# Kernel optimization log

Measured on AMD Instinct MI355X. Metric: run time of the kernel, lower is better.

Reference implementation:

```python
import jax, jax.numpy as jnp
import numpy as np

D_MODEL = 1024
NUM_HEADS = 16
HEAD_DIM = D_MODEL // NUM_HEADS
WINDOW = 64
GLOBAL_TOKENS = 4
MAX_SEQ_LEN = 2048
RANDOM_TOKENS = 32
BATCH = 2
SEQ = 2048
NEG = -1.0e9
LN_EPS = 1e-5


def setup_inputs() -> dict:
    key = jax.random.key(0)
    k1, k2, k3, k4 = jax.random.split(key, 4)
    x = jax.random.normal(k1, (BATCH, SEQ, D_MODEL), dtype=jnp.float32)
    w_qkv = jax.random.normal(k2, (D_MODEL, 3 * D_MODEL), dtype=jnp.float32) * (D_MODEL ** -0.5)
    w_out = jax.random.normal(k3, (D_MODEL, D_MODEL), dtype=jnp.float32) * (D_MODEL ** -0.5)
    ln_gamma = jnp.ones((D_MODEL,), dtype=jnp.float32)
    ln_beta = jnp.zeros((D_MODEL,), dtype=jnp.float32)
    rand_idx = jax.random.randint(k4, (MAX_SEQ_LEN, RANDOM_TOKENS), 0, MAX_SEQ_LEN, dtype=jnp.int32)
    return {"x": x, "w_qkv": w_qkv, "w_out": w_out,
            "ln_gamma": ln_gamma, "ln_beta": ln_beta, "rand_idx": rand_idx}


def _build_masks(seq_len, rand_idx):
    i = jnp.arange(seq_len)
    causal = (i[:, None] >= i[None, :]).astype(jnp.float32)  # [L,L], lower-triangular
    # local window mask
    dist = jnp.abs(i[:, None] - i[None, :])
    local = (dist <= WINDOW).astype(jnp.float32) * causal
    # global column mask: columns {0..G-1} u {L-G..L-1}, rows i >= g (== causal on those cols)
    gcols = jnp.concatenate([jnp.arange(GLOBAL_TOKENS), jnp.arange(seq_len - GLOBAL_TOKENS, seq_len)])
    is_gcol = jnp.zeros((seq_len,), jnp.float32).at[gcols].set(1.0)
    glob = is_gcol[None, :] * causal
    # random mask: per-row fixed random columns, then causal-filtered
    ri = rand_idx[:seq_len]  # [L, R]
    rows = jnp.broadcast_to(i[:, None], ri.shape)
    rnd = jnp.zeros((seq_len, seq_len), jnp.float32).at[rows, ri].set(1.0) * causal
    return local, glob, rnd


def reference(x, w_qkv, w_out, ln_gamma, ln_beta, rand_idx):
    B, L, _ = x.shape
    residual = x
    # LayerNorm
    mu = jnp.mean(x, axis=-1, keepdims=True)
    var = jnp.mean(jnp.square(x - mu), axis=-1, keepdims=True)
    xn = (x - mu) * jax.lax.rsqrt(var + LN_EPS) * ln_gamma + ln_beta
    # QKV projection
    qkv = xn @ w_qkv
    q, k, v = jnp.split(qkv, 3, axis=-1)
    q = q.reshape(B, L, NUM_HEADS, HEAD_DIM).transpose(0, 2, 1, 3)  # [B,H,L,D]
    k = k.reshape(B, L, NUM_HEADS, HEAD_DIM).transpose(0, 2, 1, 3)
    v = v.reshape(B, L, NUM_HEADS, HEAD_DIM).transpose(0, 2, 1, 3)
    local, glob, rnd = _build_masks(L, rand_idx)
    raw = jnp.einsum('bhqd,bhkd->bhqk', q, k) / jnp.sqrt(jnp.float32(HEAD_DIM))
    # original sums three masked copies of the same scores:
    # combined = 3*raw + ((1-local)+(1-glob)+(1-rnd)) * NEG
    penalty = (3.0 - (local + glob + rnd)) * NEG  # [L,L]
    combined = 3.0 * raw + penalty[None, None, :, :]
    attn = jax.nn.softmax(combined, axis=-1)
    out = jnp.einsum('bhqk,bhkd->bhqd', attn, v)
    out = out.transpose(0, 2, 1, 3).reshape(B, L, D_MODEL)
    out = out @ w_out
    return out + residual
```

## Files before the change

kernel.cpp:

```cpp
#include <hip/hip_runtime.h>
#include <stdint.h>

typedef __attribute__((ext_vector_type(8))) short shortx8;
typedef __attribute__((ext_vector_type(4))) float floatx4;

static constexpr int SEQ_    = 2048;
static constexpr int DMODEL  = 1024;
static constexpr int HDIM    = 64;
static constexpr int BATCH_  = 2;
static constexpr int NHEADS  = 16;
static constexpr int WINDOW_ = 64;
static constexpr int GTOK    = 4;
static constexpr int RTOK    = 32;
static constexpr int ROWS    = BATCH_ * SEQ_;
static constexpr int QKVN    = 3 * DMODEL;

__device__ inline unsigned short f2bf(float f) {
  union { float f; unsigned int u; } x; x.f = f;
  unsigned int r = (x.u + 0x7FFFu + ((x.u >> 16) & 1u)) >> 16;
  return (unsigned short)r;
}
__device__ inline float bf2f(unsigned short b) {
  union { unsigned int u; float f; } x; x.u = ((unsigned int)b) << 16;
  return x.f;
}

__device__ inline void gload_lds16(const void* g, void* l) {
  __builtin_amdgcn_global_load_lds(
      (const __attribute__((address_space(1))) void*)g,
      (__attribute__((address_space(3))) void*)l, 16, 0, 0);
}

__device__ __forceinline__ void gemm_core_k1024(
    const unsigned short* __restrict__ aSrc0, const unsigned short* __restrict__ aSrc1,
    const unsigned short* __restrict__ bSrc,
    unsigned short* Al, unsigned short* Bl,
    const int wave, const int lane, floatx4 (&acc)[4][2]) {
  const int quad = lane >> 4, l16 = lane & 15;
  const int wm = (wave >> 1) * 64, wn = (wave & 1) * 32;
  unsigned short* AlD0 = Al + (wave * 32) * 32;
  unsigned short* AlD1 = Al + (wave * 32 + 16) * 32;
  unsigned short* BlD  = Bl + (wave * 16) * 32;
  for (int k0 = 0; k0 < 1024; k0 += 32) {
    __syncthreads();
    gload_lds16(aSrc0 + k0, AlD0);
    gload_lds16(aSrc1 + k0, AlD1);
    gload_lds16(bSrc  + k0, BlD);
    __syncthreads();
    shortx8 af[4], bfr[2];
    #pragma unroll
    for (int s = 0; s < 4; s++)
      af[s] = *(const shortx8*)&Al[(wm + s * 16 + l16) * 32 + quad * 8];
    #pragma unroll
    for (int s = 0; s < 2; s++)
      bfr[s] = *(const shortx8*)&Bl[(wn + s * 16 + l16) * 32 + quad * 8];
    #pragma unroll
    for (int sm = 0; sm < 4; sm++)
      #pragma unroll
      for (int sn = 0; sn < 2; sn++)
        acc[sm][sn] = __builtin_amdgcn_mfma_f32_16x16x32_bf16(af[sm], bfr[sn], acc[sm][sn], 0, 0, 0);
  }
}

__global__ __launch_bounds__(256) void k1_prep(
    const float* __restrict__ x, const float* __restrict__ w_qkv,
    const float* __restrict__ w_out, const float* __restrict__ gamma,
    const float* __restrict__ beta, const int* __restrict__ ridx,
    unsigned short* __restrict__ xn, unsigned short* __restrict__ wqT,
    unsigned short* __restrict__ woT, unsigned short* __restrict__ Wvs,
    int* __restrict__ cols, int* __restrict__ cnt, int* __restrict__ tmx,
    int* __restrict__ cnts2, int* __restrict__ qlist) {
  __shared__ float tile[32][33];
  __shared__ float red[4], red2[4];
  __shared__ int rl[RTOK];
  __shared__ int scw, scnw, stm;
  const int bx = blockIdx.x;
  const int t = threadIdx.x;
  if (bx < 3072) {
    int n0 = (bx % 96) * 32, k0 = (bx / 96) * 32;
    int tx = t & 31, ty = t >> 5;
    #pragma unroll
    for (int r = ty; r < 32; r += 8)
      tile[r][tx] = w_qkv[(size_t)(k0 + r) * QKVN + n0 + tx];
    __syncthreads();
    #pragma unroll
    for (int r = ty; r < 32; r += 8)
      wqT[(size_t)(n0 + r) * DMODEL + k0 + tx] = f2bf(tile[tx][r]);
  } else if (bx < 7168) {
    int row = bx - 3072;
    const float4* xr = (const float4*)(x + (size_t)row * DMODEL);
    float4 v = xr[t];
    float s = v.x + v.y + v.z + v.w;
    #pragma unroll
    for (int o = 32; o > 0; o >>= 1) s += __shfl_xor(s, o);
    int wave = t >> 6, lane = t & 63;
    if (lane == 0) red[wave] = s;
    __syncthreads();
    float mean = (red[0] + red[1] + red[2] + red[3]) * (1.0f / DMODEL);
    float dx = v.x - mean, dy = v.y - mean, dz = v.z - mean, dw = v.w - mean;
    float q = dx*dx + dy*dy + dz*dz + dw*dw;
    #pragma unroll
    for (int o = 32; o > 0; o >>= 1) q += __shfl_xor(q, o);
    if (lane == 0) red2[wave] = q;
    __syncthreads();
    float var = (red2[0] + red2[1] + red2[2] + red2[3]) * (1.0f / DMODEL);
    float rs = rsqrtf(var + 1e-5f);
    float4 g = ((const float4*)gamma)[t];
    float4 bb = ((const float4*)beta)[t];
    ushort4 outv;
    outv.x = f2bf(dx * rs * g.x + bb.x);
    outv.y = f2bf(dy * rs * g.y + bb.y);
    outv.z = f2bf(dz * rs * g.z + bb.z);
    outv.w = f2bf(dw * rs * g.w + bb.w);
    ((ushort4*)(xn + (size_t)row * DMODEL))[t] = outv;
  } else if (bx < 8192) {
    int idx = bx - 7168;
    int n0 = (idx & 31) * 32, k0 = (idx >> 5) * 32;
    int tx = t & 31, ty = t >> 5;
    #pragma unroll
    for (int r = ty; r < 32; r += 8)
      tile[r][tx] = w_out[(size_t)(k0 + r) * DMODEL + n0 + tx];
    __syncthreads();
    #pragma unroll
    for (int r = ty; r < 32; r += 8)
      woT[(size_t)(n0 + r) * DMODEL + k0 + tx] = f2bf(tile[tx][r]);
  } else if (bx < 9216) {
    int idx = bx - 8192;
    int v0 = (idx & 31) * 32, k0 = (idx >> 5) * 32;
    int tx = t & 31, ty = t >> 5;
    #pragma unroll
    for (int r = ty; r < 32; r += 8)
      Wvs[(size_t)(k0 + r) * DMODEL + v0 + tx] =
          f2bf(w_qkv[(size_t)(k0 + r) * QKVN + 2 * DMODEL + v0 + tx]);
  } else {
    const int i = bx - 9216;
    if (t < RTOK) rl[t] = ridx[i * RTOK + t];
    if (t == 0) { scw = 0; scnw = 0; stm = 0; }
    __syncthreads();
    const int wstart = (i - WINDOW_ > 0) ? (i - WINDOW_) : 0;
    const int c = t;
    int j = -1;
    bool valid = false;
    bool iswin = (c < 65);
    if (c < 65) {
      j = i - WINDOW_ + c;
      valid = (j >= 0);
    } else if (c < 73) {
      int g = c - 65;
      j = (g < 4) ? g : (SEQ_ - 8 + g);
      valid = (j <= i) && (j < wstart);
    } else if (c < 73 + RTOK) {
      int r = c - 73;
      j = rl[r];
      bool dup = false;
      for (int r2 = 0; r2 < r; r2++) dup = dup || (rl[r2] == j);
      valid = (j <= i) && (j < wstart) && !(j < GTOK || j >= SEQ_ - GTOK) && !dup;
    }
    int tier = -1;
    if (valid) {
      int loc = ((i - j) <= WINDOW_) ? 1 : 0;
      int glb = (j < GTOK || j >= SEQ_ - GTOK) ? 1 : 0;
      int rnd = 0;
      for (int r = 0; r < RTOK; r++) rnd |= (rl[r] == j) ? 1 : 0;
      tier = loc + glb + rnd;
      atomicMax(&stm, tier);
    }
    __syncthreads();
    const int tm = stm;
    if (valid && tier == tm) {
      if (iswin) {
        int pos = atomicAdd(&scw, 1);
        cols[i * 128 + pos] = j;
      } else {
        int pos = 127 - atomicAdd(&scnw, 1);
        cols[i * 128 + pos] = j;
      }
    }
    __syncthreads();
    if (t == 0) {
      cnt[i] = scw + scnw;
      tmx[i] = tm;
      cnts2[i] = scw | (scnw << 16);
      if (i < 68 || i >= SEQ_ - 4) {
        int cc = (i < 68) ? i : 68 + (i - (SEQ_ - 4));
        qlist[cc * 2 + 0] = (tm == 3) ? i : -1;
        qlist[cc * 2 + 1] = (tm == 3) ? (SEQ_ + i) : -1;
      }
    }
  }
}

__global__ __launch_bounds__(256) void k2_wgemm(
    const unsigned short* __restrict__ woT, const unsigned short* __restrict__ Wvs,
    unsigned short* __restrict__ WvoT, const unsigned short* __restrict__ xn,
    const unsigned short* __restrict__ wqT, const int* __restrict__ qlist,
    unsigned short* __restrict__ qf, unsigned short* __restrict__ kf,
    unsigned short* __restrict__ vf) {
  __shared__ unsigned short Al[128 * 32];
  __shared__ unsigned short Bl[64 * 32];
  const int bx = blockIdx.x, t = threadIdx.x;
  const int wave = t >> 6, lane = t & 63;
  const int lrow = lane >> 2, lkoff = (lane & 3) * 8;
  const int quad = lane >> 4, l16 = lane & 15;
  const int wm = (wave >> 1) * 64, wn = (wave & 1) * 32;
  floatx4 acc[4][2] = {};
  if (bx < 128) {
    const int bm = (bx >> 4) * 128, bn = (bx & 15) * 64;
    const unsigned short* a0 = woT + (size_t)(bm + wave * 32 + lrow) * DMODEL + lkoff;
    const unsigned short* a1 = a0 + 16 * DMODEL;
    const unsigned short* b0 = Wvs + (size_t)(bn + wave * 16 + lrow) * DMODEL + lkoff;
    gemm_core_k1024(a0, a1, b0, Al, Bl, wave, lane, acc);
    #pragma unroll
    for (int sm = 0; sm < 4; sm++)
      #pragma unroll
      for (int sn = 0; sn < 2; sn++)
        #pragma unroll
        for (int r = 0; r < 4; r++) {
          int row = bm + wm + sm * 16 + quad * 4 + r;
          int col = bn + wn + sn * 16 + l16;
          WvoT[(size_t)row * DMODEL + col] = f2bf(acc[sm][sn][r]);
        }
  } else {
    const int idx = bx - 128;
    const int job = idx >> 4, bn = (idx & 15) * 64;
    const int wsel = (job < 2) ? 0 : ((job == 2) ? 1 : 2);
    const unsigned short* BT = wqT + (size_t)wsel * DMODEL * DMODEL;
    unsigned short* dstbuf = (job == 0) ? qf
                           : (job == 1) ? (qf + (size_t)128 * DMODEL)
                           : (job == 2) ? kf : vf;
    int rsrc[2];
    #pragma unroll
    for (int q = 0; q < 2; q++) {
      int m = wave * 32 + q * 16 + lrow;
      int row;
      if (job < 2) {
        int s = job * 128 + m;
        int ql = (s < 144) ? qlist[s] : -1;
        row = (ql < 0) ? 0 : ql;
      } else {
        row = (m < 16) ? ((m >> 3) * SEQ_ + (((m & 7) < 4) ? (m & 7) : (SEQ_ - 8 + (m & 7)))) : 0;
      }
      rsrc[q] = row;
    }
    const unsigned short* a0 = xn + (size_t)rsrc[0] * DMODEL + lkoff;
    const unsigned short* a1 = xn + (size_t)rsrc[1] * DMODEL + lkoff;
    const unsigned short* b0 = BT + (size_t)(bn + wave * 16 + lrow) * DMODEL + lkoff;
    gemm_core_k1024(a0, a1, b0, Al, Bl, wave, lane, acc);
    #pragma unroll
    for (int sm = 0; sm < 4; sm++)
      #pragma unroll
      for (int sn = 0; sn < 2; sn++)
        #pragma unroll
        for (int r = 0; r < 4; r++) {
          int m = wm + sm * 16 + quad * 4 + r;
          int col = bn + wn + sn * 16 + l16;
          dstbuf[(size_t)m * DMODEL + col] = f2bf(acc[sm][sn][r]);
        }
  }
}

__global__ __launch_bounds__(256) void k3_xbar(
    const unsigned short* __restrict__ xn, const int* __restrict__ cols,
    const int* __restrict__ cnt, const int* __restrict__ tmx,
    const int* __restrict__ cnts2, const int* __restrict__ qlist,
    const unsigned short* __restrict__ qf, const unsigned short* __restrict__ kf,
    const unsigned short* __restrict__ vf,
    unsigned short* __restrict__ xbar, unsigned short* __restrict__ vbar) {
  const int bx = blockIdx.x, t = threadIdx.x;
  const int wave = t >> 6, lane = t & 63;
  if (bx < 1024) {
    __shared__ unsigned short win[80][256];
    const int b = bx >> 9, rest = bx & 511;
    const int i0 = (rest >> 2) * 16, dimbase = (rest & 3) * 256;
    const size_t xnb = (size_t)(b * SEQ_) * DMODEL;
    const int lo = i0 - 64;
    const int r0 = i0 + wave * 4;
    int tm_[4], cw_[4], cnw_[4], jr0_[4], jr1_[4];
    #pragma unroll
    for (int rr = 0; rr < 4; rr++) {
      const int i = r0 + rr;
      tm_[rr] = tmx[i];
      int c2 = cnts2[i];
      cw_[rr] = c2 & 0xffff; cnw_[rr] = c2 >> 16;
      jr0_[rr] = cols[i * 128 + lane];
      jr1_[rr] = cols[i * 128 + 64 + lane];
    }
    {
      const int l5 = lane & 31, rsub = lane >> 5;
      #pragma unroll 5
      for (int it = 0; it < 10; it++) {
        int r = it * 8 + wave * 2 + rsub;
        int gr = lo + r;
        if (gr >= 0)
          *(int4*)&win[r][l5 * 8] =
              *(const int4*)(xn + xnb + (size_t)gr * DMODEL + dimbase + l5 * 8);
      }
    }
    __syncthreads();
    const unsigned short* xnd = xn + xnb + dimbase + lane * 4;
    auto add4 = [](float4& s, ushort4 v) {
      s.x += bf2f(v.x); s.y += bf2f(v.y); s.z += bf2f(v.z); s.w += bf2f(v.w);
    };
    auto sub4 = [](float4& s, ushort4 v) {
      s.x -= bf2f(v.x); s.y -= bf2f(v.y); s.z -= bf2f(v.z); s.w -= bf2f(v.w);
    };
    float4 ws = {0, 0, 0, 0};
    {
      float4 t1 = {0,0,0,0}, t2 = {0,0,0,0}, t3 = {0,0,0,0};
      const int jstart = (r0 - 64 > 0) ? (r0 - 64) : 0;
      const int cn = r0 - jstart + 1;
      const int base = jstart - lo;
      int c = 0;
      for (; c + 4 <= cn; c += 4) {
        ushort4 v0 = *(const ushort4*)&win[base + c][lane * 4];
        ushort4 v1 = *(const ushort4*)&win[base + c + 1][lane * 4];
        ushort4 v2 = *(const ushort4*)&win[base + c + 2][lane * 4];
        ushort4 v3 = *(const ushort4*)&win[base + c + 3][lane * 4];
        add4(ws, v0); add4(t1, v1); add4(t2, v2); add4(t3, v3);
      }
      for (; c < cn; c++) add4(ws, *(const ushort4*)&win[base + c][lane * 4]);
      ws.x += t1.x + t2.x + t3.x; ws.y += t1.y + t2.y + t3.y;
      ws.z += t1.z + t2.z + t3.z; ws.w += t1.w + t2.w + t3.w;
    }
    for (int rr = 0; rr < 4; rr++) {
      const int i = r0 + rr;
      if (rr > 0) {
        add4(ws, *(const ushort4*)&win[i - lo][lane * 4]);
        int dj = i - 65;
        if (dj >= 0) sub4(ws, *(const ushort4*)&win[dj - lo][lane * 4]);
      }
      const int tm = tm_[rr];
      ushort4 o;
      if (tm == 3) {
        o.x = o.y = o.z = o.w = 0;
      } else {
        const int cw = cw_[rr], cnw = cnw_[rr];
        const int jr1 = jr1_[rr];
        float4 s;
        if (tm == 1) {
          s = ws;
          float4 t1 = {0,0,0,0}, t2 = {0,0,0,0}, t3 = {0,0,0,0};
          const int bb = 64 - cnw;
          int c = 0;
          for (; c + 8 <= cnw; c += 8) {
            ushort4 v0 = *(const ushort4*)(xnd + (size_t)__shfl(jr1, bb + c)     * DMODEL);
            ushort4 v1 = *(const ushort4*)(xnd + (size_t)__shfl(jr1, bb + c + 1) * DMODEL);
            ushort4 v2 = *(const ushort4*)(xnd + (size_t)__shfl(jr1, bb + c + 2) * DMODEL);
            ushort4 v3 = *(const ushort4*)(xnd + (size_t)__shfl(jr1, bb + c + 3) * DMODEL);
            ushort4 v4 = *(const ushort4*)(xnd + (size_t)__shfl(jr1, bb + c + 4) * DMODEL);
            ushort4 v5 = *(const ushort4*)(xnd + (size_t)__shfl(jr1, bb + c + 5) * DMODEL);
            ushort4 v6 = *(const ushort4*)(xnd + (size_t)__shfl(jr1, bb + c + 6) * DMODEL);
            ushort4 v7 = *(const ushort4*)(xnd + (size_t)__shfl(jr1, bb + c + 7) * DMODEL);
            add4(s, v0); add4(t1, v1); add4(t2, v2); add4(t3, v3);
            add4(s, v4); add4(t1, v5); add4(t2, v6); add4(t3, v7);
          }
          if (c + 4 <= cnw) {
            ushort4 v0 = *(const ushort4*)(xnd + (size_t)__shfl(jr1, bb + c)     * DMODEL);
            ushort4 v1 = *(const ushort4*)(xnd + (size_t)__shfl(jr1, bb + c + 1) * DMODEL);
            ushort4 v2 = *(const ushort4*)(xnd + (size_t)__shfl(jr1, bb + c + 2) * DMODEL);
            ushort4 v3 = *(const ushort4*)(xnd + (size_t)__shfl(jr1, bb + c + 3) * DMODEL);
            add4(s, v0); add4(t1, v1); add4(t2, v2); add4(t3, v3);
            c += 4;
          }
          for (; c < cnw; c++)
            add4(s, *(const ushort4*)(xnd + (size_t)__shfl(jr1, bb + c) * DMODEL));
          s.x += t1.x + t2.x + t3.x; s.y += t1.y + t2.y + t3.y;
          s.z += t1.z + t2.z + t3.z; s.w += t1.w + t2.w + t3.w;
        } else {
          const int jr0 = jr0_[rr];
          s.x = s.y = s.z = s.w = 0.f;
          for (int c = 0; c < cw; c++) {
            int j = (c < 64) ? __shfl(jr0, c) : __shfl(jr1, c - 64);
            add4(s, *(const ushort4*)(xnd + (size_t)j * DMODEL));
          }
          const int bb = 64 - cnw;
          for (int c = 0; c < cnw; c++)
            add4(s, *(const ushort4*)(xnd + (size_t)__shfl(jr1, bb + c) * DMODEL));
        }
        const float inv = 1.0f / (float)(cw + cnw);
        o.x = f2bf(s.x * inv); o.y = f2bf(s.y * inv);
        o.z = f2bf(s.z * inv); o.w = f2bf(s.w * inv);
      }
      *(ushort4*)(xbar + (size_t)(b * SEQ_ + i) * DMODEL + dimbase + lane * 4) = o;
    }
  } else {
    const int s = (bx - 1024) * 4 + wave;
    const int dst = (s < 144) ? qlist[s] : -1;
    if (dst < 0) return;
    const int b = dst >> 11, i = dst & (SEQ_ - 1);
    const int n = cnt[i];
    int myk = 0;
    if (lane < n) {
      int kj = cols[i * 128 + lane];
      myk = b * 8 + ((kj < 4) ? kj : (kj - (SEQ_ - 8)));
    }
    for (int h = 0; h < NHEADS; h++) {
      float qd = bf2f(qf[(size_t)s * DMODEL + h * HDIM + lane]);
      float w[8];
      float m = -1e30f;
      for (int c = 0; c < n; c++) {
        int ks = __shfl(myk, c);
        float kd = bf2f(kf[(size_t)ks * DMODEL + h * HDIM + lane]);
        float p = qd * kd;
        #pragma unroll
        for (int o = 32; o > 0; o >>= 1) p += __shfl_xor(p, o);
        p *= 0.375f;
        w[c] = p;
        m = fmaxf(m, p);
      }
      float denom = 0.f, acc = 0.f;
      for (int c = 0; c < n; c++) {
        int ks = __shfl(myk, c);
        float e = __expf(w[c] - m);
        denom += e;
        acc += e * bf2f(vf[(size_t)ks * DMODEL + h * HDIM + lane]);
      }
      vbar[(size_t)s * DMODEL + h * HDIM + lane] = f2bf(acc / denom);
    }
  }
}

__global__ __launch_bounds__(256) void k4_final(
    const unsigned short* __restrict__ xbar, const unsigned short* __restrict__ WvoT,
    const unsigned short* __restrict__ vbar, const unsigned short* __restrict__ woT,
    const int* __restrict__ qlist, const int* __restrict__ tmx,
    const float* __restrict__ x, float* __restrict__ out) {
  __shared__ unsigned short Al[128 * 32];
  __shared__ unsigned short Bl[64 * 32];
  __shared__ int rowinf[128];
  const int bx = blockIdx.x, t = threadIdx.x;
  const int wave = t >> 6, lane = t & 63;
  const int lrow = lane >> 2, lkoff = (lane & 3) * 8;
  const int quad = lane >> 4, l16 = lane & 15;
  const int wm = (wave >> 1) * 64, wn = (wave & 1) * 32;
  floatx4 acc[4][2] = {};
  if (bx < 512) {
    const int bm = (bx >> 4) * 128, bn = (bx & 15) * 64;
    if (t < 128) rowinf[t] = tmx[(bm + t) & (SEQ_ - 1)];
    const unsigned short* a0 = xbar + (size_t)(bm + wave * 32 + lrow) * DMODEL + lkoff;
    const unsigned short* a1 = a0 + 16 * DMODEL;
    const unsigned short* b0 = WvoT + (size_t)(bn + wave * 16 + lrow) * DMODEL + lkoff;
    gemm_core_k1024(a0, a1, b0, Al, Bl, wave, lane, acc);
    #pragma unroll
    for (int sm = 0; sm < 4; sm++)
      #pragma unroll
      for (int sn = 0; sn < 2; sn++)
        #pragma unroll
        for (int r = 0; r < 4; r++) {
          int m = wm + sm * 16 + quad * 4 + r;
          if (rowinf[m] != 3) {
            int col = bn + wn + sn * 16 + l16;
            size_t off = (size_t)(bm + m) * DMODEL + col;
            out[off] = acc[sm][sn][r] + x[off];
          }
        }
  } else {
    const int idx = bx - 512;
    const int bm = (idx >> 4) * 128, bn = (idx & 15) * 64;
    if (t < 128) {
      int s = bm + t;
      rowinf[t] = (s < 144) ? qlist[s] : -1;
    }
    const unsigned short* a0 = vbar + (size_t)(bm + wave * 32 + lrow) * DMODEL + lkoff;
    const unsigned short* a1 = a0 + 16 * DMODEL;
    const unsigned short* b0 = woT + (size_t)(bn + wave * 16 + lrow) * DMODEL + lkoff;
    gemm_core_k1024(a0, a1, b0, Al, Bl, wave, lane, acc);
    #pragma unroll
    for (int sm = 0; sm < 4; sm++)
      #pragma unroll
      for (int sn = 0; sn < 2; sn++)
        #pragma unroll
        for (int r = 0; r < 4; r++) {
          int m = wm + sm * 16 + quad * 4 + r;
          int dst = rowinf[m];
          if (dst >= 0) {
            int col = bn + wn + sn * 16 + l16;
            size_t off = (size_t)dst * DMODEL + col;
            out[off] = acc[sm][sn][r] + x[off];
          }
        }
  }
}

extern "C" void kernel_launch(void* const* d_in, const int* in_sizes, int n_in,
                              void* d_out, int out_size, void* d_ws, size_t ws_size,
                              hipStream_t stream) {
  const float* x     = (const float*)d_in[0];
  const float* w_qkv = (const float*)d_in[1];
  const float* w_out = (const float*)d_in[2];
  const float* gamma = (const float*)d_in[3];
  const float* beta  = (const float*)d_in[4];
  const int*   ridx  = (const int*)d_in[5];
  float* out = (float*)d_out;

  char* ws = (char*)d_ws;
  size_t off = 0;
  auto alloc = [&](size_t bytes) {
    char* p = ws + off;
    off = (off + bytes + 255) & ~(size_t)255;
    return p;
  };
  unsigned short* xn   = (unsigned short*)alloc((size_t)ROWS * DMODEL * 2);
  unsigned short* wqT  = (unsigned short*)alloc((size_t)QKVN * DMODEL * 2);
  unsigned short* woT  = (unsigned short*)alloc((size_t)DMODEL * DMODEL * 2);
  unsigned short* Wvs  = (unsigned short*)alloc((size_t)DMODEL * DMODEL * 2);
  unsigned short* WvoT = (unsigned short*)alloc((size_t)DMODEL * DMODEL * 2);
  unsigned short* xbar = (unsigned short*)alloc((size_t)ROWS * DMODEL * 2);
  unsigned short* qf   = (unsigned short*)alloc((size_t)256 * DMODEL * 2);
  unsigned short* kf   = (unsigned short*)alloc((size_t)128 * DMODEL * 2);
  unsigned short* vf   = (unsigned short*)alloc((size_t)128 * DMODEL * 2);
  unsigned short* vbar = (unsigned short*)alloc((size_t)256 * DMODEL * 2);
  int* cols  = (int*)alloc((size_t)SEQ_ * 128 * 4);
  int* cnt   = (int*)alloc((size_t)SEQ_ * 4);
  int* tmx   = (int*)alloc((size_t)SEQ_ * 4);
  int* cnts2 = (int*)alloc((size_t)SEQ_ * 4);
  int* qlist = (int*)alloc(256 * 4);

  hipLaunchKernelGGL(k1_prep, dim3(11264), dim3(256), 0, stream,
                     x, w_qkv, w_out, gamma, beta, ridx,
                     xn, wqT, woT, Wvs, cols, cnt, tmx, cnts2, qlist);
  hipLaunchKernelGGL(k2_wgemm, dim3(192), dim3(256), 0, stream,
                     woT, Wvs, WvoT, xn, wqT, qlist, qf, kf, vf);
  hipLaunchKernelGGL(k3_xbar, dim3(1060), dim3(256), 0, stream,
                     xn, cols, cnt, tmx, cnts2, qlist, qf, kf, vf, xbar, vbar);
  hipLaunchKernelGGL(k4_final, dim3(544), dim3(256), 0, stream,
                     xbar, WvoT, vbar, woT, qlist, tmx, x, out);
}
```

Before: 168.4 us.

## Merge weight GEMM kernel into xbar kernel and move global-row attention into final kernel

Removes the separate k2 launch by folding the Wvo and global-row Q/K/V GEMM blocks into extra blocks of the xbar kernel. The sparse global-query attention that produced vbar moves into the final kernel's vbar-GEMM blocks, which compute vbar first and then fence and sync before consuming it. It also skips the sliding-window sum when none of a wave's rows need it. This saves one launch and its dependency barrier, but the final kernel's 32 extra blocks now carry serial attention work before their GEMM, which could lengthen the tail.

```diff
diff --git a/kernel.cpp b/kernel.cpp
--- a/kernel.cpp
+++ b/kernel.cpp
@@ -190,82 +190,15 @@
   }
 }
 
-__global__ __launch_bounds__(256) void k2_wgemm(
-    const unsigned short* __restrict__ woT, const unsigned short* __restrict__ Wvs,
-    unsigned short* __restrict__ WvoT, const unsigned short* __restrict__ xn,
-    const unsigned short* __restrict__ wqT, const int* __restrict__ qlist,
-    unsigned short* __restrict__ qf, unsigned short* __restrict__ kf,
-    unsigned short* __restrict__ vf) {
-  __shared__ unsigned short Al[128 * 32];
-  __shared__ unsigned short Bl[64 * 32];
-  const int bx = blockIdx.x, t = threadIdx.x;
-  const int wave = t >> 6, lane = t & 63;
-  const int lrow = lane >> 2, lkoff = (lane & 3) * 8;
-  const int quad = lane >> 4, l16 = lane & 15;
-  const int wm = (wave >> 1) * 64, wn = (wave & 1) * 32;
-  floatx4 acc[4][2] = {};
-  if (bx < 128) {
-    const int bm = (bx >> 4) * 128, bn = (bx & 15) * 64;
-    const unsigned short* a0 = woT + (size_t)(bm + wave * 32 + lrow) * DMODEL + lkoff;
-    const unsigned short* a1 = a0 + 16 * DMODEL;
-    const unsigned short* b0 = Wvs + (size_t)(bn + wave * 16 + lrow) * DMODEL + lkoff;
-    gemm_core_k1024(a0, a1, b0, Al, Bl, wave, lane, acc);
-    #pragma unroll
-    for (int sm = 0; sm < 4; sm++)
-      #pragma unroll
-      for (int sn = 0; sn < 2; sn++)
-        #pragma unroll
-        for (int r = 0; r < 4; r++) {
-          int row = bm + wm + sm * 16 + quad * 4 + r;
-          int col = bn + wn + sn * 16 + l16;
-          WvoT[(size_t)row * DMODEL + col] = f2bf(acc[sm][sn][r]);
-        }
-  } else {
-    const int idx = bx - 128;
-    const int job = idx >> 4, bn = (idx & 15) * 64;
-    const int wsel = (job < 2) ? 0 : ((job == 2) ? 1 : 2);
-    const unsigned short* BT = wqT + (size_t)wsel * DMODEL * DMODEL;
-    unsigned short* dstbuf = (job == 0) ? qf
-                           : (job == 1) ? (qf + (size_t)128 * DMODEL)
-                           : (job == 2) ? kf : vf;
-    int rsrc[2];
-    #pragma unroll
-    for (int q = 0; q < 2; q++) {
-      int m = wave * 32 + q * 16 + lrow;
-      int row;
-      if (job < 2) {
-        int s = job * 128 + m;
-        int ql = (s < 144) ? qlist[s] : -1;
-        row = (ql < 0) ? 0 : ql;
-      } else {
-        row = (m < 16) ? ((m >> 3) * SEQ_ + (((m & 7) < 4) ? (m & 7) : (SEQ_ - 8 + (m & 7)))) : 0;
-      }
-      rsrc[q] = row;
-    }
-    const unsigned short* a0 = xn + (size_t)rsrc[0] * DMODEL + lkoff;
-    const unsigned short* a1 = xn + (size_t)rsrc[1] * DMODEL + lkoff;
-    const unsigned short* b0 = BT + (size_t)(bn + wave * 16 + lrow) * DMODEL + lkoff;
-    gemm_core_k1024(a0, a1, b0, Al, Bl, wave, lane, acc);
-    #pragma unroll
-    for (int sm = 0; sm < 4; sm++)
-      #pragma unroll
-      for (int sn = 0; sn < 2; sn++)
-        #pragma unroll
-        for (int r = 0; r < 4; r++) {
-          int m = wm + sm * 16 + quad * 4 + r;
-          int col = bn + wn + sn * 16 + l16;
-          dstbuf[(size_t)m * DMODEL + col] = f2bf(acc[sm][sn][r]);
-        }
-  }
-}
-
 __global__ __launch_bounds__(256) void k3_xbar(
     const unsigned short* __restrict__ xn, const int* __restrict__ cols,
     const int* __restrict__ cnt, const int* __restrict__ tmx,
     const int* __restrict__ cnts2, const int* __restrict__ qlist,
-    const unsigned short* __restrict__ qf, const unsigned short* __restrict__ kf,
-    const unsigned short* __restrict__ vf,
-    unsigned short* __restrict__ xbar, unsigned short* __restrict__ vbar) {
+    const unsigned short* __restrict__ woT, const unsigned short* __restrict__ Wvs,
+    const unsigned short* __restrict__ wqT,
+    unsigned short* __restrict__ WvoT, unsigned short* __restrict__ qf,
+    unsigned short* __restrict__ kf, unsigned short* __restrict__ vf,
+    unsigned short* __restrict__ xbar) {
   const int bx = blockIdx.x, t = threadIdx.x;
   const int wave = t >> 6, lane = t & 63;
   if (bx < 1024) {
@@ -285,6 +218,7 @@
       jr0_[rr] = cols[i * 128 + lane];
       jr1_[rr] = cols[i * 128 + 64 + lane];
     }
+    const bool needws = (tm_[0] == 1) | (tm_[1] == 1) | (tm_[2] == 1) | (tm_[3] == 1);
     {
       const int l5 = lane & 31, rsub = lane >> 5;
       #pragma unroll 5
@@ -305,7 +239,7 @@
       s.x -= bf2f(v.x); s.y -= bf2f(v.y); s.z -= bf2f(v.z); s.w -= bf2f(v.w);
     };
     float4 ws = {0, 0, 0, 0};
-    {
+    if (needws) {
       float4 t1 = {0,0,0,0}, t2 = {0,0,0,0}, t3 = {0,0,0,0};
       const int jstart = (r0 - 64 > 0) ? (r0 - 64) : 0;
       const int cn = r0 - jstart + 1;
@@ -324,7 +258,7 @@
     }
     for (int rr = 0; rr < 4; rr++) {
       const int i = r0 + rr;
-      if (rr > 0) {
+      if (needws && rr > 0) {
         add4(ws, *(const ushort4*)&win[i - lo][lane * 4]);
         int dj = i - 65;
         if (dj >= 0) sub4(ws, *(const ushort4*)&win[dj - lo][lane * 4]);
@@ -384,45 +318,75 @@
       *(ushort4*)(xbar + (size_t)(b * SEQ_ + i) * DMODEL + dimbase + lane * 4) = o;
     }
   } else {
-    const int s = (bx - 1024) * 4 + wave;
-    const int dst = (s < 144) ? qlist[s] : -1;
-    if (dst < 0) return;
-    const int b = dst >> 11, i = dst & (SEQ_ - 1);
-    const int n = cnt[i];
-    int myk = 0;
-    if (lane < n) {
-      int kj = cols[i * 128 + lane];
-      myk = b * 8 + ((kj < 4) ? kj : (kj - (SEQ_ - 8)));
-    }
-    for (int h = 0; h < NHEADS; h++) {
-      float qd = bf2f(qf[(size_t)s * DMODEL + h * HDIM + lane]);
-      float w[8];
-      float m = -1e30f;
-      for (int c = 0; c < n; c++) {
-        int ks = __shfl(myk, c);
-        float kd = bf2f(kf[(size_t)ks * DMODEL + h * HDIM + lane]);
-        float p = qd * kd;
+    __shared__ unsigned short Al[128 * 32];
+    __shared__ unsigned short Bl[64 * 32];
+    const int lrow = lane >> 2, lkoff = (lane & 3) * 8;
+    const int quad = lane >> 4, l16 = lane & 15;
+    const int wm = (wave >> 1) * 64, wn = (wave & 1) * 32;
+    floatx4 acc[4][2] = {};
+    if (bx < 1152) {
+      const int idx = bx - 1024;
+      const int bm = (idx >> 4) * 128, bn = (idx & 15) * 64;
+      const unsigned short* a0 = woT + (size_t)(bm + wave * 32 + lrow) * DMODEL + lkoff;
+      const unsigned short* a1 = a0 + 16 * DMODEL;
+      const unsigned short* b0 = Wvs + (size_t)(bn + wave * 16 + lrow) * DMODEL + lkoff;
+      gemm_core_k1024(a0, a1, b0, Al, Bl, wave, lane, acc);
+      #pragma unroll
+      for (int sm = 0; sm < 4; sm++)
         #pragma unroll
-        for (int o = 32; o > 0; o >>= 1) p += __shfl_xor(p, o);
-        p *= 0.375f;
-        w[c] = p;
-        m = fmaxf(m, p);
-      }
-      float denom = 0.f, acc = 0.f;
-      for (int c = 0; c < n; c++) {
-        int ks = __shfl(myk, c);
-        float e = __expf(w[c] - m);
-        denom += e;
-        acc += e * bf2f(vf[(size_t)ks * DMODEL + h * HDIM + lane]);
-      }
-      vbar[(size_t)s * DMODEL + h * HDIM + lane] = f2bf(acc / denom);
+        for (int sn = 0; sn < 2; sn++)
+          #pragma unroll
+          for (int r = 0; r < 4; r++) {
+            int row = bm + wm + sm * 16 + quad * 4 + r;
+            int col = bn + wn + sn * 16 + l16;
+            WvoT[(size_t)row * DMODEL + col] = f2bf(acc[sm][sn][r]);
+          }
+    } else {
+      const int idx = bx - 1152;
+      const int job = idx >> 4, bn = (idx & 15) * 64;
+      const int wsel = (job < 2) ? 0 : ((job == 2) ? 1 : 2);
+      const unsigned short* BT = wqT + (size_t)wsel * DMODEL * DMODEL;
+      unsigned short* dstbuf = (job == 0) ? qf
+                             : (job == 1) ? (qf + (size_t)128 * DMODEL)
+                             : (job == 2) ? kf : vf;
+      int rsrc[2];
+      #pragma unroll
+      for (int q = 0; q < 2; q++) {
+        int m = wave * 32 + q * 16 + lrow;
+        int row;
+        if (job < 2) {
+          int s = job * 128 + m;
+          int ql = (s < 144) ? qlist[s] : -1;
+          row = (ql < 0) ? 0 : ql;
+        } else {
+          row = (m < 16) ? ((m >> 3) * SEQ_ + (((m & 7) < 4) ? (m & 7) : (SEQ_ - 8 + (m & 7)))) : 0;
+        }
+        rsrc[q] = row;
+      }
+      const unsigned short* a0 = xn + (size_t)rsrc[0] * DMODEL + lkoff;
+      const unsigned short* a1 = xn + (size_t)rsrc[1] * DMODEL + lkoff;
+      const unsigned short* b0 = BT + (size_t)(bn + wave * 16 + lrow) * DMODEL + lkoff;
+      gemm_core_k1024(a0, a1, b0, Al, Bl, wave, lane, acc);
+      #pragma unroll
+      for (int sm = 0; sm < 4; sm++)
+        #pragma unroll
+        for (int sn = 0; sn < 2; sn++)
+          #pragma unroll
+          for (int r = 0; r < 4; r++) {
+            int m = wm + sm * 16 + quad * 4 + r;
+            int col = bn + wn + sn * 16 + l16;
+            dstbuf[(size_t)m * DMODEL + col] = f2bf(acc[sm][sn][r]);
+          }
     }
   }
 }
 
 __global__ __launch_bounds__(256) void k4_final(
     const unsigned short* __restrict__ xbar, const unsigned short* __restrict__ WvoT,
-    const unsigned short* __restrict__ vbar, const unsigned short* __restrict__ woT,
+    const unsigned short* __restrict__ woT,
+    const unsigned short* __restrict__ qf, const unsigned short* __restrict__ kf,
+    const unsigned short* __restrict__ vf, unsigned short* __restrict__ vbar,
+    const int* __restrict__ cols, const int* __restrict__ cnt,
     const int* __restrict__ qlist, const int* __restrict__ tmx,
     const float* __restrict__ x, float* __restrict__ out) {
   __shared__ unsigned short Al[128 * 32];
@@ -457,6 +421,43 @@
   } else {
     const int idx = bx - 512;
     const int bm = (idx >> 4) * 128, bn = (idx & 15) * 64;
+    for (int s4 = wave; s4 < 128; s4 += 4) {
+      const int s = bm + s4;
+      const int dst = (s < 144) ? qlist[s] : -1;
+      if (dst < 0) continue;
+      const int b = dst >> 11, i = dst & (SEQ_ - 1);
+      const int n = cnt[i];
+      int myk = 0;
+      if (lane < n) {
+        int kj = cols[i * 128 + lane];
+        myk = b * 8 + ((kj < 4) ? kj : (kj - (SEQ_ - 8)));
+      }
+      for (int h = 0; h < NHEADS; h++) {
+        float qd = bf2f(qf[(size_t)s * DMODEL + h * HDIM + lane]);
+        float w[8];
+        float m = -1e30f;
+        for (int c = 0; c < n; c++) {
+          int ks = __shfl(myk, c);
+          float kd = bf2f(kf[(size_t)ks * DMODEL + h * HDIM + lane]);
+          float p = qd * kd;
+          #pragma unroll
+          for (int o = 32; o > 0; o >>= 1) p += __shfl_xor(p, o);
+          p *= 0.375f;
+          w[c] = p;
+          m = fmaxf(m, p);
+        }
+        float denom = 0.f, accv = 0.f;
+        for (int c = 0; c < n; c++) {
+          int ks = __shfl(myk, c);
+          float e = __expf(w[c] - m);
+          denom += e;
+          accv += e * bf2f(vf[(size_t)ks * DMODEL + h * HDIM + lane]);
+        }
+        vbar[(size_t)s * DMODEL + h * HDIM + lane] = f2bf(accv / denom);
+      }
+    }
+    __threadfence();
+    __syncthreads();
     if (t < 128) {
       int s = bm + t;
       rowinf[t] = (s < 144) ? qlist[s] : -1;
@@ -519,10 +520,9 @@
   hipLaunchKernelGGL(k1_prep, dim3(11264), dim3(256), 0, stream,
                      x, w_qkv, w_out, gamma, beta, ridx,
                      xn, wqT, woT, Wvs, cols, cnt, tmx, cnts2, qlist);
-  hipLaunchKernelGGL(k2_wgemm, dim3(192), dim3(256), 0, stream,
-                     woT, Wvs, WvoT, xn, wqT, qlist, qf, kf, vf);
-  hipLaunchKernelGGL(k3_xbar, dim3(1060), dim3(256), 0, stream,
-                     xn, cols, cnt, tmx, cnts2, qlist, qf, kf, vf, xbar, vbar);
+  hipLaunchKernelGGL(k3_xbar, dim3(1216), dim3(256), 0, stream,
+                     xn, cols, cnt, tmx, cnts2, qlist, woT, Wvs, wqT,
+                     WvoT, qf, kf, vf, xbar);
   hipLaunchKernelGGL(k4_final, dim3(544), dim3(256), 0, stream,
-                     xbar, WvoT, vbar, woT, qlist, tmx, x, out);
-}
+                     xbar, WvoT, woT, qf, kf, vf, vbar, cols, cnt, qlist, tmx, x, out);
+}
```

Measured after the change: 197.6 us. 17.4% more time.
